# Kernel tuning notes

Hardware: AMD Instinct MI355X
Metric: run time of the kernel (lower is better)

## Reference

```python
import jax, jax.numpy as jnp
import numpy as np

STRIDE = 1
PAD = 1
KH = KW = 3


def setup_inputs() -> dict:
    key = jax.random.key(0)
    k1, k2, k3, k4 = jax.random.split(key, 4)
    B, Cin, H, W = 4, 64, 128, 128
    Cout = 64
    x = jax.random.normal(k1, (B, Cin, H, W), jnp.float32)
    # offset conv params (zero-init in original; small random so offsets are nontrivial)
    ow = jax.random.normal(k2, (3, Cin, KH, KW), jnp.float32) * 0.01
    ob = jax.random.normal(k3, (3,), jnp.float32) * 0.1
    weight = jax.random.normal(k4, (Cout, Cin, KH, KW), jnp.float32)
    return {"x": x, "ow": ow, "ob": ob, "weight": weight}


def _build_offset(o):
    # o: [B,3,H,W] -> 3-DoF constrained offsets (translation dy,dx + rotation r)
    oy, ox, orr = o[:, 0:1], o[:, 1:2], o[:, 2:3]
    oyp1 = oy + 1.0
    oxp1 = ox + 1.0
    s = jnp.sin(orr)
    c = jnp.cos(orr)
    one = jnp.ones_like(oy)
    zero = jnp.zeros_like(oy)
    offy = jnp.concatenate([
        -oxp1 * s - oyp1 * c + one, -oxp1 * s, -oxp1 * s + oyp1 * c - one,
        -oyp1 * c + one, zero, oyp1 * c - one,
        oxp1 * s - oyp1 * c + one, oxp1 * s, oxp1 * s + oyp1 * c - one,
    ], axis=1)
    offx = jnp.concatenate([
        -oxp1 * c + oyp1 * s + one, -oxp1 * c + one, -oxp1 * c - oyp1 * s + one,
        oyp1 * s, zero, -oyp1 * s,
        oxp1 * c + oyp1 * s - one, oxp1 * c - one, oxp1 * c - oyp1 * s - one,
    ], axis=1)
    return jnp.concatenate([offy, offx], axis=1)  # [B,18,H,W]


def _deform_conv2d(x, offset, weight):
    # torchvision semantics: offset channels are interleaved (dy_k, dx_k) per kernel tap k
    B, C, H, W = x.shape
    OC = weight.shape[0]
    K = KH * KW
    Ho = (H + 2 * PAD - KH) // STRIDE + 1
    Wo = (W + 2 * PAD - KW) // STRIDE + 1
    off = offset.reshape(B, K, 2, Ho, Wo)
    ky = jnp.repeat(jnp.arange(KH), KW).astype(x.dtype)  # [K] row-major kernel taps
    kx = jnp.tile(jnp.arange(KW), KH).astype(x.dtype)
    base_y = (jnp.arange(Ho) * STRIDE - PAD).astype(x.dtype)
    base_x = (jnp.arange(Wo) * STRIDE - PAD).astype(x.dtype)
    py = base_y[None, None, :, None] + ky[None, :, None, None] + off[:, :, 0]  # [B,K,Ho,Wo]
    px = base_x[None, None, None, :] + kx[None, :, None, None] + off[:, :, 1]
    y0 = jnp.floor(py)
    x0 = jnp.floor(px)
    wy1 = py - y0
    wy0 = 1.0 - wy1
    wx1 = px - x0
    wx0 = 1.0 - wx1
    xf = x.reshape(B, C, H * W)

    def gather(yi, xi):
        valid = ((yi >= 0) & (yi < H) & (xi >= 0) & (xi < W)).astype(x.dtype)
        yc = jnp.clip(yi, 0, H - 1).astype(jnp.int32)
        xc = jnp.clip(xi, 0, W - 1).astype(jnp.int32)
        idx = (yc * W + xc).reshape(B, 1, K * Ho * Wo)
        v = jnp.take_along_axis(xf, idx, axis=2).reshape(B, C, K, Ho, Wo)
        return v * valid[:, None]

    sampled = (gather(y0, x0) * (wy0 * wx0)[:, None]
               + gather(y0, x0 + 1.0) * (wy0 * wx1)[:, None]
               + gather(y0 + 1.0, x0) * (wy1 * wx0)[:, None]
               + gather(y0 + 1.0, x0 + 1.0) * (wy1 * wx1)[:, None])  # [B,C,K,Ho,Wo]
    return jnp.einsum('bckhw,ock->bohw', sampled, weight.reshape(OC, C, K))


def reference(x, ow, ob, weight):
    o = jax.lax.conv_general_dilated(
        x, ow, window_strides=(STRIDE, STRIDE), padding=((PAD, PAD), (PAD, PAD)),
        dimension_numbers=('NCHW', 'OIHW', 'NCHW')) + ob[None, :, None, None]
    offset = _build_offset(o)
    return _deform_conv2d(x, offset, weight)
```

## Files before the change

### kernel.cpp

```cpp
#include <hip/hip_runtime.h>

#define H 128
#define W 128
#define HW 16384
#define C 64
#define NOC 64
#define NB 4

__global__ __launch_bounds__(256) void transpose_x(const float* __restrict__ x,
                                                   float* __restrict__ xT) {
    __shared__ float T[64 * 64];
    int blk = blockIdx.x;
    int b = blk >> 8;
    int hw0 = (blk & 255) << 6;
    int t = threadIdx.x;

    const float* xb = x + ((size_t)b * C) * HW + hw0;
    int cl = t >> 4;
    int wl = (t & 15) << 2;
#pragma unroll
    for (int rep = 0; rep < 4; ++rep) {
        int c = cl + (rep << 4);
        float4 v = *(const float4*)(xb + (size_t)c * HW + wl);
        float vv[4] = {v.x, v.y, v.z, v.w};
#pragma unroll
        for (int j = 0; j < 4; ++j) {
            int w = wl + j;
            int g = (w >> 2) & 7;
            T[w * 64 + (c ^ (g << 2))] = vv[j];
        }
    }
    __syncthreads();
    float* xTb = xT + ((size_t)b * HW + hw0) * C;
    int wr = t >> 4;
    int cr = (t & 15) << 2;
#pragma unroll
    for (int rep = 0; rep < 4; ++rep) {
        int w = wr + (rep << 4);
        int g = (w >> 2) & 7;
        float4 v = *(const float4*)(&T[w * 64 + (cr ^ (g << 2))]);
        *(float4*)(xTb + (size_t)w * C + cr) = v;
    }
}

__global__ __launch_bounds__(256) void offset_kernel(const float* __restrict__ xT,
                                                     const float* __restrict__ ow,
                                                     const float* __restrict__ ob,
                                                     float2* __restrict__ taps) {
    __shared__ float ows[3 * 64 * 9];
    __shared__ float tile[16][18 * 18];
    int t = threadIdx.x;
    int tx = t & 15, ty = t >> 4;
    for (int i = t; i < 1728; i += 256) ows[i] = ow[i];

    int b = blockIdx.z;
    int y0 = blockIdx.y * 16, x0 = blockIdx.x * 16;
    int gy = y0 + ty, gx = x0 + tx;
    float acc0 = ob[0], acc1 = ob[1], acc2 = ob[2];
    const float* xb = xT + (size_t)b * HW * C;

#pragma unroll 1
    for (int cc = 0; cc < 4; ++cc) {
        int cbase = cc << 4;
        __syncthreads();
        for (int i = t; i < 1296; i += 256) {
            int px = i >> 2, cq = i & 3;
            int iy = px / 18, ix = px - iy * 18;
            int yy = y0 - 1 + iy, xx = x0 - 1 + ix;
            float4 v = make_float4(0.f, 0.f, 0.f, 0.f);
            if (yy >= 0 && yy < H && xx >= 0 && xx < W)
                v = *(const float4*)(xb + (((size_t)(yy * W + xx)) << 6) + cbase + (cq << 2));
            tile[(cq << 2) + 0][px] = v.x;
            tile[(cq << 2) + 1][px] = v.y;
            tile[(cq << 2) + 2][px] = v.z;
            tile[(cq << 2) + 3][px] = v.w;
        }
        __syncthreads();
#pragma unroll 2
        for (int c = 0; c < 16; ++c) {
            const float* owc = &ows[(cbase + c) * 9];
            const float* trow = &tile[c][0];
#pragma unroll
            for (int dy = 0; dy < 3; ++dy)
#pragma unroll
                for (int dx = 0; dx < 3; ++dx) {
                    float v = trow[(ty + dy) * 18 + tx + dx];
                    int kk = dy * 3 + dx;
                    acc0 += v * owc[kk];
                    acc1 += v * owc[576 + kk];
                    acc2 += v * owc[1152 + kk];
                }
        }
    }

    float oyp1 = acc0 + 1.f, oxp1 = acc1 + 1.f;
    float sn = sinf(acc2), cs = cosf(acc2);
    float A = oxp1 * sn, Bc = oyp1 * cs, Cs = oyp1 * sn, D = oxp1 * cs;
    float offc[18];
    offc[0] = -A - Bc + 1.f;  offc[1] = -A;        offc[2] = -A + Bc - 1.f;
    offc[3] = -Bc + 1.f;      offc[4] = 0.f;       offc[5] = Bc - 1.f;
    offc[6] = A - Bc + 1.f;   offc[7] = A;         offc[8] = A + Bc - 1.f;
    offc[9] = -D + Cs + 1.f;  offc[10] = -D + 1.f; offc[11] = -D - Cs + 1.f;
    offc[12] = Cs;            offc[13] = 0.f;      offc[14] = -Cs;
    offc[15] = D + Cs - 1.f;  offc[16] = D - 1.f;  offc[17] = D - Cs - 1.f;

    int pix = gy * W + gx;
#pragma unroll
    for (int k = 0; k < 9; ++k) {
        float py = (float)(gy - 1 + k / 3) + offc[2 * k];
        float px = (float)(gx - 1 + k % 3) + offc[2 * k + 1];
        taps[((size_t)b * 9 + k) * HW + pix] = make_float2(py, px);
    }
}

__global__ __launch_bounds__(256) void reorder_w(const float* __restrict__ w,
                                                 float* __restrict__ wt) {
    int idx = blockIdx.x * 256 + threadIdx.x;
    if (idx >= NOC * C * 9) return;
    int oc = idx & 63;
    int rest = idx >> 6;
    int c = rest & 63;
    int k = rest >> 6;
    wt[idx] = w[((size_t)oc * C + c) * 9 + k];
}

__global__ __launch_bounds__(256, 2) void deform_gemm(const float* __restrict__ xT,
                                                      const float2* __restrict__ taps,
                                                      const float* __restrict__ wt,
                                                      float* __restrict__ out) {
    __shared__ float S[C * 128];
    __shared__ float Wl[C * NOC];
    __shared__ float metaF[128 * 4];
    __shared__ int   metaI[128 * 4];
    int t = threadIdx.x;
    int orig = blockIdx.x;
    int blk = ((orig & 7) << 6) + (orig >> 3);
    int b = blk >> 7;
    int pix0 = (blk & 127) << 7;
    const float* xb = xT + (size_t)b * HW * C;
    const float2* tb = taps + (size_t)b * 9 * HW;

    float acc[8][4];
#pragma unroll
    for (int i = 0; i < 8; ++i)
#pragma unroll
        for (int j = 0; j < 4; ++j) acc[i][j] = 0.f;

    int c0 = (t & 15) << 2;
    int pg16 = t >> 4;
    int ocg = t & 15;
    int p0 = (t >> 4) << 3;

    auto compute_meta = [&](int k) {
        if (t < 128) {
            float2 pp = tb[(size_t)k * HW + pix0 + t];
            float y0f = floorf(pp.x), x0f = floorf(pp.y);
            float fy = pp.x - y0f, fx = pp.y - x0f;
            int iy0 = (int)y0f, ix0 = (int)x0f;
            int iy1 = iy0 + 1, ix1 = ix0 + 1;
            bool vy0 = (iy0 >= 0) & (iy0 < H), vy1 = (iy1 >= 0) & (iy1 < H);
            bool vx0 = (ix0 >= 0) & (ix0 < W), vx1 = (ix1 >= 0) & (ix1 < W);
            float w00 = (vy0 & vx0) ? (1.f - fy) * (1.f - fx) : 0.f;
            float w01 = (vy0 & vx1) ? (1.f - fy) * fx : 0.f;
            float w10 = (vy1 & vx0) ? fy * (1.f - fx) : 0.f;
            float w11 = (vy1 & vx1) ? fy * fx : 0.f;
            int cy0 = min(max(iy0, 0), H - 1), cy1 = min(max(iy1, 0), H - 1);
            int cx0 = min(max(ix0, 0), W - 1), cx1 = min(max(ix1, 0), W - 1);
            *(float4*)&metaF[t << 2] = make_float4(w00, w01, w10, w11);
            *(int4*)&metaI[t << 2] = make_int4((cy0 * W + cx0) << 6, (cy0 * W + cx1) << 6,
                                               (cy1 * W + cx0) << 6, (cy1 * W + cx1) << 6);
        }
    };

    compute_meta(0);

#pragma unroll 1
    for (int k = 0; k < 9; ++k) {
        __syncthreads();
        {
            const float4* wsrc = (const float4*)(wt + k * 4096);
            float4* wdst = (float4*)Wl;
#pragma unroll
            for (int i = 0; i < 4; ++i) wdst[t + 256 * i] = wsrc[t + 256 * i];
        }
#pragma unroll 2
        for (int it = 0; it < 8; ++it) {
            int p = (it << 4) + pg16;
            float4 wv = *(const float4*)&metaF[p << 2];
            int4 ov = *(const int4*)&metaI[p << 2];
            float4 a00 = *(const float4*)(xb + ov.x + c0);
            float4 a01 = *(const float4*)(xb + ov.y + c0);
            float4 a10 = *(const float4*)(xb + ov.z + c0);
            float4 a11 = *(const float4*)(xb + ov.w + c0);
            float sv0 = wv.x * a00.x + wv.y * a01.x + wv.z * a10.x + wv.w * a11.x;
            float sv1 = wv.x * a00.y + wv.y * a01.y + wv.z * a10.y + wv.w * a11.y;
            float sv2 = wv.x * a00.z + wv.y * a01.z + wv.z * a10.z + wv.w * a11.z;
            float sv3 = wv.x * a00.w + wv.y * a01.w + wv.z * a10.w + wv.w * a11.w;
            float svv[4] = {sv0, sv1, sv2, sv3};
#pragma unroll
            for (int j = 0; j < 4; ++j) {
                int c = c0 + j;
                S[(c << 7) + (p ^ (((c >> 2) & 7) << 2))] = svv[j];
            }
        }
        __syncthreads();
#pragma unroll 4
        for (int c = 0; c < C; ++c) {
            float4 wv = *(const float4*)(Wl + (c << 6) + (ocg << 2));
            int xk = ((c >> 2) & 7) << 2;
            const float* srow = S + (c << 7);
            float4 slo = *(const float4*)(srow + (p0 ^ xk));
            float4 shi = *(const float4*)(srow + ((p0 + 4) ^ xk));
            float sp[8] = {slo.x, slo.y, slo.z, slo.w, shi.x, shi.y, shi.z, shi.w};
#pragma unroll
            for (int ip = 0; ip < 8; ++ip) {
                acc[ip][0] += sp[ip] * wv.x;
                acc[ip][1] += sp[ip] * wv.y;
                acc[ip][2] += sp[ip] * wv.z;
                acc[ip][3] += sp[ip] * wv.w;
            }
        }
        if (k < 8) compute_meta(k + 1);
    }

    __syncthreads();
#pragma unroll
    for (int ip = 0; ip < 8; ++ip) {
        int p = p0 + ip;
#pragma unroll
        for (int j = 0; j < 4; ++j) {
            int oc = (ocg << 2) + j;
            S[(oc << 7) + (p ^ (((oc >> 2) & 7) << 2))] = acc[ip][j];
        }
    }
    __syncthreads();
    float* ob_ = out + ((size_t)b * NOC) * HW + pix0;
#pragma unroll
    for (int rep = 0; rep < 2; ++rep) {
        int oc = (t >> 3) + (rep << 5);
        int xk = ((oc >> 2) & 7) << 2;
        int pxb = (t & 7) << 4;
        const float* srow = S + (oc << 7);
#pragma unroll
        for (int q = 0; q < 4; ++q) {
            int p = pxb + (q << 2);
            float4 v = *(const float4*)(srow + (p ^ xk));
            *(float4*)(ob_ + (size_t)oc * HW + p) = v;
        }
    }
}

extern "C" void kernel_launch(void* const* d_in, const int* in_sizes, int n_in,
                              void* d_out, int out_size, void* d_ws, size_t ws_size,
                              hipStream_t stream) {
    const float* x = (const float*)d_in[0];
    const float* ow = (const float*)d_in[1];
    const float* ob = (const float*)d_in[2];
    const float* w = (const float*)d_in[3];
    float* out = (float*)d_out;

    char* ws = (char*)d_ws;
    float* xT = (float*)ws;
    float2* taps = (float2*)(ws + (size_t)16777216);
    float* wt = (float*)(ws + (size_t)16777216 + 4718592);

    hipLaunchKernelGGL(transpose_x, dim3(NB * 256), dim3(256), 0, stream, x, xT);
    hipLaunchKernelGGL(reorder_w, dim3(144), dim3(256), 0, stream, w, wt);
    hipLaunchKernelGGL(offset_kernel, dim3(8, 8, NB), dim3(256), 0, stream,
                       xT, ow, ob, taps);
    hipLaunchKernelGGL(deform_gemm, dim3(NB * 128), dim3(256), 0, stream,
                       xT, taps, wt, out);
}
```

Baseline: 187.8 us.

## Remap offset conv to 16 lanes per pixel with shuffle reduction

```diff
diff --git a/kernel.cpp b/kernel.cpp
--- a/kernel.cpp
+++ b/kernel.cpp
@@ -47,69 +47,61 @@
                                                      const float* __restrict__ ow,
                                                      const float* __restrict__ ob,
                                                      float2* __restrict__ taps) {
-    __shared__ float ows[3 * 64 * 9];
-    __shared__ float tile[16][18 * 18];
+    __shared__ float ows[1728];
     int t = threadIdx.x;
-    int tx = t & 15, ty = t >> 4;
     for (int i = t; i < 1728; i += 256) ows[i] = ow[i];
-
-    int b = blockIdx.z;
-    int y0 = blockIdx.y * 16, x0 = blockIdx.x * 16;
-    int gy = y0 + ty, gx = x0 + tx;
-    float acc0 = ob[0], acc1 = ob[1], acc2 = ob[2];
-    const float* xb = xT + (size_t)b * HW * C;
-
-#pragma unroll 1
-    for (int cc = 0; cc < 4; ++cc) {
-        int cbase = cc << 4;
-        __syncthreads();
-        for (int i = t; i < 1296; i += 256) {
-            int px = i >> 2, cq = i & 3;
-            int iy = px / 18, ix = px - iy * 18;
-            int yy = y0 - 1 + iy, xx = x0 - 1 + ix;
-            float4 v = make_float4(0.f, 0.f, 0.f, 0.f);
-            if (yy >= 0 && yy < H && xx >= 0 && xx < W)
-                v = *(const float4*)(xb + (((size_t)(yy * W + xx)) << 6) + cbase + (cq << 2));
-            tile[(cq << 2) + 0][px] = v.x;
-            tile[(cq << 2) + 1][px] = v.y;
-            tile[(cq << 2) + 2][px] = v.z;
-            tile[(cq << 2) + 3][px] = v.w;
-        }
-        __syncthreads();
-#pragma unroll 2
-        for (int c = 0; c < 16; ++c) {
-            const float* owc = &ows[(cbase + c) * 9];
-            const float* trow = &tile[c][0];
-#pragma unroll
-            for (int dy = 0; dy < 3; ++dy)
-#pragma unroll
-                for (int dx = 0; dx < 3; ++dx) {
-                    float v = trow[(ty + dy) * 18 + tx + dx];
-                    int kk = dy * 3 + dx;
-                    acc0 += v * owc[kk];
-                    acc1 += v * owc[576 + kk];
-                    acc2 += v * owc[1152 + kk];
-                }
-        }
-    }
-
-    float oyp1 = acc0 + 1.f, oxp1 = acc1 + 1.f;
-    float sn = sinf(acc2), cs = cosf(acc2);
-    float A = oxp1 * sn, Bc = oyp1 * cs, Cs = oyp1 * sn, D = oxp1 * cs;
-    float offc[18];
-    offc[0] = -A - Bc + 1.f;  offc[1] = -A;        offc[2] = -A + Bc - 1.f;
-    offc[3] = -Bc + 1.f;      offc[4] = 0.f;       offc[5] = Bc - 1.f;
-    offc[6] = A - Bc + 1.f;   offc[7] = A;         offc[8] = A + Bc - 1.f;
-    offc[9] = -D + Cs + 1.f;  offc[10] = -D + 1.f; offc[11] = -D - Cs + 1.f;
-    offc[12] = Cs;            offc[13] = 0.f;      offc[14] = -Cs;
-    offc[15] = D + Cs - 1.f;  offc[16] = D - 1.f;  offc[17] = D - Cs - 1.f;
-
-    int pix = gy * W + gx;
+    float b0 = ob[0], b1 = ob[1], b2 = ob[2];
+    __syncthreads();
+
+    int gid = blockIdx.x * 256 + t;
+    int gp = gid >> 4;
+    int cg = t & 15;
+    int b = gp >> 14;
+    int pix = gp & 16383;
+    int gy = pix >> 7, gx = pix & 127;
+
+    const float* xb = xT + (((size_t)b) << 14) * C;
+    float acc0 = 0.f, acc1 = 0.f, acc2 = 0.f;
 #pragma unroll
     for (int k = 0; k < 9; ++k) {
-        float py = (float)(gy - 1 + k / 3) + offc[2 * k];
-        float px = (float)(gx - 1 + k % 3) + offc[2 * k + 1];
-        taps[((size_t)b * 9 + k) * HW + pix] = make_float2(py, px);
+        const int dy = k / 3 - 1, dx = k % 3 - 1;
+        int yy = gy + dy, xx = gx + dx;
+        bool valid = (yy >= 0) & (yy < H) & (xx >= 0) & (xx < W);
+        int cy = min(max(yy, 0), H - 1), cx = min(max(xx, 0), W - 1);
+        float4 v = *(const float4*)(xb + (((size_t)(cy * W + cx)) << 6) + (cg << 2));
+        float m = valid ? 1.f : 0.f;
+        float vj[4] = {v.x * m, v.y * m, v.z * m, v.w * m};
+        const float* wp = &ows[(cg << 2) * 9 + k];
+#pragma unroll
+        for (int j = 0; j < 4; ++j) {
+            acc0 += vj[j] * wp[j * 9];
+            acc1 += vj[j] * wp[576 + j * 9];
+            acc2 += vj[j] * wp[1152 + j * 9];
+        }
+    }
+#pragma unroll
+    for (int s = 1; s < 16; s <<= 1) {
+        acc0 += __shfl_xor(acc0, s);
+        acc1 += __shfl_xor(acc1, s);
+        acc2 += __shfl_xor(acc2, s);
+    }
+    acc0 += b0; acc1 += b1; acc2 += b2;
+
+    if (cg < 9) {
+        float oyp1 = acc0 + 1.f, oxp1 = acc1 + 1.f;
+        float sn = sinf(acc2), cs = cosf(acc2);
+        float A = oxp1 * sn, Bc = oyp1 * cs, Cs = oyp1 * sn, D = oxp1 * cs;
+        auto chval = [&](int m) {
+            int j = (m < 9) ? m : m - 9;
+            float jy = (float)(j / 3 - 1), jx = (float)(j % 3 - 1);
+            return (m < 9) ? (jy * A + jx * (Bc - 1.f))
+                           : (jy * (D - 1.f) - jx * Cs);
+        };
+        int ky = (cg >= 6) ? 2 : ((cg >= 3) ? 1 : 0);
+        int kx = cg - ky * 3;
+        float py = (float)(gy + ky - 1) + chval(2 * cg);
+        float px = (float)(gx + kx - 1) + chval(2 * cg + 1);
+        taps[(((size_t)b * 9 + cg) << 14) + pix] = make_float2(py, px);
     }
 }
 
@@ -266,7 +258,7 @@
 
     hipLaunchKernelGGL(transpose_x, dim3(NB * 256), dim3(256), 0, stream, x, xT);
     hipLaunchKernelGGL(reorder_w, dim3(144), dim3(256), 0, stream, w, wt);
-    hipLaunchKernelGGL(offset_kernel, dim3(8, 8, NB), dim3(256), 0, stream,
+    hipLaunchKernelGGL(offset_kernel, dim3(4096), dim3(256), 0, stream,
                        xT, ow, ob, taps);
     hipLaunchKernelGGL(deform_gemm, dim3(NB * 128), dim3(256), 0, stream,
                        xT, taps, wt, out);
```

Measured after the change: 178.2 us. 1.05x faster.
